# Kernel tuning notes

Hardware: AMD Instinct MI355X
Metric: run time of the kernel (lower is better)

## Reference

```python
import jax, jax.numpy as jnp
import numpy as np

EPS = 1e-5

def _batchnorm(x, gamma, beta):
    # x: [N, C, T]; training-mode BN: batch stats over (N, T) per channel
    mean = jnp.mean(x, axis=(0, 2), keepdims=True)
    var = jnp.mean((x - mean) ** 2, axis=(0, 2), keepdims=True)
    xhat = (x - mean) * jax.lax.rsqrt(var + EPS)
    return xhat * gamma[None, :, None] + beta[None, :, None]

def _temporal_shift(x, s):
    # x: [N, C, T], s: [C] learnable per-channel shift (Shift-GCN style)
    # out[n,c,t] = linear interp of x[n,c, t + s[c]], zero outside [0, T)
    N, C, T = x.shape
    pos = jnp.arange(T, dtype=x.dtype)[None, :] + s[:, None]  # [C, T]
    i0f = jnp.floor(pos)
    frac = pos - i0f                                          # [C, T]
    i0 = i0f.astype(jnp.int32)
    i1 = i0 + 1
    v0 = ((i0 >= 0) & (i0 < T)).astype(x.dtype)
    v1 = ((i1 >= 0) & (i1 < T)).astype(x.dtype)
    cidx = jnp.arange(C)[:, None]                             # [C, 1]
    g0 = x[:, cidx, jnp.clip(i0, 0, T - 1)]                   # [N, C, T]
    g1 = x[:, cidx, jnp.clip(i1, 0, T - 1)]
    return g0 * ((1.0 - frac) * v0) + g1 * (frac * v1)

def setup_inputs() -> dict:
    key = jax.random.key(0)
    ks = jax.random.split(key, 5)
    N, T, Cin, Cout = 128, 1024, 256, 256
    x = jax.random.normal(ks[0], (N, T, Cin), dtype=jnp.float32)
    # kaiming_normal fan_out for 1x1 conv: std = sqrt(2 / Cout)
    conv_w = jax.random.normal(ks[1], (Cout, Cin), dtype=jnp.float32) * np.sqrt(2.0 / Cout)
    conv_b = jnp.zeros((Cout,), dtype=jnp.float32)
    shift_in_s = jax.random.uniform(ks[2], (Cin,), dtype=jnp.float32, minval=-1.0, maxval=1.0)
    shift_out_s = jax.random.uniform(ks[3], (Cout,), dtype=jnp.float32, minval=-1.0, maxval=1.0)
    return {
        "x": x,
        "bn1_gamma": jnp.ones((Cin,), jnp.float32),
        "bn1_beta": jnp.zeros((Cin,), jnp.float32),
        "shift_in_s": shift_in_s,
        "conv_w": conv_w,
        "conv_b": conv_b,
        "shift_out_s": shift_out_s,
        "bn2_gamma": jnp.ones((Cout,), jnp.float32),
        "bn2_beta": jnp.zeros((Cout,), jnp.float32),
    }

def reference(x, bn1_gamma, bn1_beta, shift_in_s, conv_w, conv_b, shift_out_s, bn2_gamma, bn2_beta):
    # x: [N, T, C] -> [N, C, T] (permute; trailing singleton W dim elided)
    h = jnp.transpose(x, (0, 2, 1))
    h = _batchnorm(h, bn1_gamma, bn1_beta)
    h = _temporal_shift(h, shift_in_s)
    # 1x1 conv == per-position channel mixing
    h = jnp.einsum("nct,oc->not", h, conv_w) + conv_b[None, :, None]
    h = jax.nn.relu(h)
    h = _temporal_shift(h, shift_out_s)
    h = _batchnorm(h, bn2_gamma, bn2_beta)
    return jnp.transpose(h, (0, 2, 1))  # back to [N, T, C_out]
```

## Files before the change

### kernel.cpp

```cpp
#include <hip/hip_runtime.h>
#include <stddef.h>

typedef __attribute__((ext_vector_type(8))) short short8;
typedef __attribute__((ext_vector_type(4))) float f32x4;
typedef __attribute__((ext_vector_type(4))) int   i32x4;
typedef __attribute__((ext_vector_type(2))) unsigned int u32x2;
typedef unsigned short ushort_t;
typedef unsigned int uint_t;

#define TT 1024
#define NT 131072.0f
#define EPS 1e-5f

__device__ __forceinline__ float bf2f(ushort_t u){
    union { float f; uint_t i; } v; v.i = ((uint_t)u) << 16; return v.f;
}
__device__ __forceinline__ ushort_t f2bf(float f){
    union { float f; uint_t i; } v; v.f = f;
    uint_t r = v.i + 0x7fffu + ((v.i >> 16) & 1u);
    return (ushort_t)(r >> 16);
}
__device__ __forceinline__ uint_t pack2(float lo, float hi){
    return (uint_t)f2bf(lo) | ((uint_t)f2bf(hi) << 16);
}
__device__ __forceinline__ f32x4 ld4bf(const ushort_t* p){
    u32x2 u = *(const u32x2*)p;
    f32x4 r;
    r[0] = bf2f((ushort_t)(u[0] & 0xffffu));
    r[1] = bf2f((ushort_t)(u[0] >> 16));
    r[2] = bf2f((ushort_t)(u[1] & 0xffffu));
    r[3] = bf2f((ushort_t)(u[1] >> 16));
    return r;
}
__device__ __forceinline__ void wave_red(float& v){
    #pragma unroll
    for (int off = 32; off > 0; off >>= 1) v += __shfl_down(v, off);
}
__device__ __forceinline__ void dma16(const void* g, void* l){
    __builtin_amdgcn_global_load_lds(
        (const __attribute__((address_space(1))) unsigned int*)g,
        (__attribute__((address_space(3))) unsigned int*)l, 16, 0, 0);
}

__global__ __launch_bounds__(256) void k_prep(const float* __restrict__ x,
                                              const float* __restrict__ a0i,
                                              const float* __restrict__ a1i,
                                              const int* __restrict__ i1i,
                                              ushort_t* __restrict__ xs,
                                              float* __restrict__ psum,
                                              float* __restrict__ psq){
    __shared__ float ls[4][256], lq[4][256];
    const int b = blockIdx.x, tid = threadIdx.x;
    const int c4 = (tid & 63) << 2, rq = tid >> 6;
    const size_t row0 = ((size_t)b << 6) + ((size_t)rq << 4);
    const int n = (int)(row0 >> 10), rt = (int)(row0 & 1023);
    const float* xp = x + ((size_t)n << 18) + c4;
    ushort_t* wp = xs + ((size_t)n << 18);
    const f32x4 a0v = *(const f32x4*)&a0i[c4];
    const f32x4 a1v = *(const f32x4*)&a1i[c4];
    const i32x4 i1v = *(const i32x4*)&i1i[c4];
    f32x4 s = {0.f,0.f,0.f,0.f}, q = {0.f,0.f,0.f,0.f};
    f32x4 Bm1 = {0.f,0.f,0.f,0.f};
    if (rt > 0) Bm1 = *(const f32x4*)&xp[(size_t)(rt - 1) << 8];
    f32x4 B0 = *(const f32x4*)&xp[(size_t)rt << 8];
    #pragma unroll 8
    for (int k = 0; k < 16; ++k){
        const int t = rt + k;
        f32x4 Bp1 = {0.f,0.f,0.f,0.f};
        if (t < 1023) Bp1 = *(const f32x4*)&xp[(size_t)(t + 1) << 8];
        f32x4 v;
        #pragma unroll
        for (int j = 0; j < 4; ++j){
            s[j] += B0[j]; q[j] = fmaf(B0[j], B0[j], q[j]);
            float zl = i1v[j] ? B0[j]  : Bm1[j];
            float zr = i1v[j] ? Bp1[j] : B0[j];
            v[j] = a0v[j] * zl + a1v[j] * zr;
        }
        u32x2 u; u[0] = pack2(v[0], v[1]); u[1] = pack2(v[2], v[3]);
        *(u32x2*)&wp[((size_t)t << 8) + (c4 ^ ((t & 7) << 3))] = u;
        Bm1 = B0; B0 = Bp1;
    }
    #pragma unroll
    for (int j = 0; j < 4; ++j){ ls[rq][c4 + j] = s[j]; lq[rq][c4 + j] = q[j]; }
    __syncthreads();
    const int c = tid;
    psum[(size_t)b * 256 + c] = ls[0][c] + ls[1][c] + ls[2][c] + ls[3][c];
    psq [(size_t)b * 256 + c] = lq[0][c] + lq[1][c] + lq[2][c] + lq[3][c];
}

__global__ __launch_bounds__(256) void k_shift(const float* __restrict__ sin_,
                                               const float* __restrict__ sout,
                                               float* __restrict__ a0i, float* __restrict__ a1i,
                                               int* __restrict__ i1i,
                                               float* __restrict__ a0o, float* __restrict__ a1o,
                                               int* __restrict__ j1o){
    const int c = blockIdx.x * 256 + threadIdx.x;
    if (c < 256){
        float sv = sin_[c]; float fi = floorf(sv); float fr = sv - fi;
        a0i[c] = 1.f - fr; a1i[c] = fr; i1i[c] = (int)fi + 1;
        float so = sout[c]; float fo = floorf(so); float fro = so - fo;
        a0o[c] = 1.f - fro; a1o[c] = fro; j1o[c] = (int)fo + 1;
    }
}

__global__ __launch_bounds__(256) void k_fin1(const float* __restrict__ psum,
                                              const float* __restrict__ psq,
                                              const float* __restrict__ g1,
                                              const float* __restrict__ be1,
                                              float* __restrict__ s1, float* __restrict__ b1){
    const int c = blockIdx.x, t = threadIdx.x;
    float s = 0.f, q = 0.f;
    #pragma unroll
    for (int i = 0; i < 8; ++i){
        const size_t b = (size_t)(t * 8 + i);
        s += psum[b * 256 + c]; q += psq[b * 256 + c];
    }
    wave_red(s); wave_red(q);
    __shared__ float sm[8];
    const int wv = t >> 6, ln = t & 63;
    if (ln == 0){ sm[wv] = s; sm[4 + wv] = q; }
    __syncthreads();
    if (t == 0){
        float S = sm[0] + sm[1] + sm[2] + sm[3];
        float Q = sm[4] + sm[5] + sm[6] + sm[7];
        float mean = S / NT;
        float var  = Q / NT - mean * mean;
        float rstd = rsqrtf(var + EPS);
        float sc = rstd * g1[c];
        s1[c] = sc;
        b1[c] = be1[c] - mean * sc;
    }
}

__global__ __launch_bounds__(256) void k_wf(const float* __restrict__ W,
                                            const float* __restrict__ s1,
                                            ushort_t* __restrict__ WF){
    const int gid = blockIdx.x * 256 + threadIdx.x;
    const int l = gid & 63, ob = (gid >> 6) & 15, ks = gid >> 10;
    const int row = ob * 16 + (l & 15);
    const int k0  = ks * 32 + (l >> 4) * 8;
    #pragma unroll
    for (int j = 0; j < 8; ++j)
        WF[(size_t)gid * 8 + j] = f2bf(W[(size_t)row * 256 + k0 + j] * s1[k0 + j]);
}

__global__ __launch_bounds__(256) void k_wb(const float* __restrict__ W,
                                            const float* __restrict__ cb,
                                            const float* __restrict__ b1,
                                            const float* __restrict__ a0i,
                                            const float* __restrict__ a1i,
                                            const int* __restrict__ i1i,
                                            float* __restrict__ bias2,
                                            float* __restrict__ corr0,
                                            float* __restrict__ corrT){
    const int o = blockIdx.x, c = threadIdx.x;
    const float w = W[(size_t)o * 256 + c];
    float wb = w * b1[c];
    float c0 = (i1i[c] == 0) ? wb * a0i[c] : 0.f;
    float cT = (i1i[c] == 1) ? wb * a1i[c] : 0.f;
    wave_red(wb); wave_red(c0); wave_red(cT);
    __shared__ float sm[4][3];
    const int wv = c >> 6, ln = c & 63;
    if (ln == 0){ sm[wv][0] = wb; sm[wv][1] = c0; sm[wv][2] = cT; }
    __syncthreads();
    if (c == 0){
        bias2[o] = cb[o] + sm[0][0] + sm[1][0] + sm[2][0] + sm[3][0];
        corr0[o] = sm[0][1] + sm[1][1] + sm[2][1] + sm[3][1];
        corrT[o] = sm[0][2] + sm[1][2] + sm[2][2] + sm[3][2];
    }
}

__global__ __launch_bounds__(256) void k_conv(const ushort_t* __restrict__ xs,
                                              const ushort_t* __restrict__ WF,
                                              const float* __restrict__ bias2,
                                              const float* __restrict__ corr0,
                                              const float* __restrict__ corrT,
                                              ushort_t* __restrict__ Y,
                                              float* __restrict__ SP, float* __restrict__ SQ,
                                              float* __restrict__ SR,
                                              float* __restrict__ FR, float* __restrict__ LR){
    __shared__ __align__(16) ushort_t lds[16384];
    const int tid = threadIdx.x;
    const int n  = blockIdx.x >> 4;
    const int t0 = (blockIdx.x & 15) << 6;
    const int lane = tid & 63, wv = tid >> 6;

    {
        const ushort_t* gsrc = xs + ((size_t)n << 18) + ((size_t)(t0 + (wv << 4)) << 8);
        #pragma unroll
        for (int i = 0; i < 8; ++i)
            dma16(gsrc + (i << 9) + (lane << 3), &lds[(wv << 12) + (i << 9)]);
    }
    __syncthreads();

    const int l15 = lane & 15, lg = lane >> 4;
    f32x4 acc[4][4];
    #pragma unroll
    for (int r = 0; r < 4; ++r)
        #pragma unroll
        for (int q = 0; q < 4; ++q)
            acc[r][q] = (f32x4){0.f, 0.f, 0.f, 0.f};

    const short8* wf8 = (const short8*)WF;
    #pragma unroll
    for (int ks = 0; ks < 8; ++ks){
        short8 aF[4], bF[4];
        #pragma unroll
        for (int r = 0; r < 4; ++r)
            aF[r] = wf8[(ks * 16 + wv * 4 + r) * 64 + lane];
        const int kk = (ks << 5) + (lg << 3);
        #pragma unroll
        for (int q = 0; q < 4; ++q){
            const int t = (q << 4) | l15;
            bF[q] = *(const short8*)&lds[(t << 8) + (kk ^ ((t & 7) << 3))];
        }
        #pragma unroll
        for (int r = 0; r < 4; ++r)
            #pragma unroll
            for (int q = 0; q < 4; ++q)
                acc[r][q] = __builtin_amdgcn_mfma_f32_16x16x32_bf16(aF[r], bF[q], acc[r][q], 0, 0, 0);
    }
    __syncthreads();

    const bool isFirst = (t0 == 0), isLast = (t0 == 960);
    #pragma unroll
    for (int r = 0; r < 4; ++r){
        const int ob = (wv << 6) + (r << 4) + (lg << 2);
        const f32x4 cbv = *(const f32x4*)&bias2[ob];
        f32x4 c0v = {0.f,0.f,0.f,0.f}, cTv = {0.f,0.f,0.f,0.f};
        if (isFirst) c0v = *(const f32x4*)&corr0[ob];
        if (isLast)  cTv = *(const f32x4*)&corrT[ob];
        #pragma unroll
        for (int q = 0; q < 4; ++q){
            const int t = (q << 4) | l15;
            float v[4];
            #pragma unroll
            for (int j = 0; j < 4; ++j){
                float z = acc[r][q][j] + cbv[j];
                if (isFirst && t == 0)  z -= c0v[j];
                if (isLast  && t == 63) z -= cTv[j];
                v[j] = z > 0.f ? z : 0.f;
            }
            u32x2 w; w[0] = pack2(v[0], v[1]); w[1] = pack2(v[2], v[3]);
            *(u32x2*)&lds[(t << 8) + (ob ^ ((t & 7) << 3))] = w;
        }
    }
    __syncthreads();

    u32x2* Yu = (u32x2*)Y;
    const size_t rbase = ((size_t)n << 10) + t0;
    #pragma unroll
    for (int it = 0; it < 16; ++it){
        const int row = (it << 2) + wv;
        u32x2 v = *(const u32x2*)&lds[(row << 8) + ((lane << 2) ^ ((row & 7) << 3))];
        Yu[((rbase + row) << 6) + lane] = v;
    }
    {
        const int o = tid;
        FR[(size_t)blockIdx.x * 256 + o] = bf2f(lds[o]);
        LR[(size_t)blockIdx.x * 256 + o] = bf2f(lds[(63 << 8) + (o ^ 56)]);
    }
    f32x4 P = {0.f,0.f,0.f,0.f}, Q = P, R = P;
    {
        const int o4 = lane << 2;
        const int r0 = wv << 4;
        f32x4 prev = {0.f,0.f,0.f,0.f};
        if (wv > 0) prev = ld4bf(&lds[((r0 - 1) << 8) + (o4 ^ (((r0 - 1) & 7) << 3))]);
        #pragma unroll 8
        for (int k = 0; k < 16; ++k){
            const int t = r0 + k;
            f32x4 y = ld4bf(&lds[(t << 8) + (o4 ^ ((t & 7) << 3))]);
            #pragma unroll
            for (int j = 0; j < 4; ++j){
                P[j] += y[j];
                Q[j] = fmaf(y[j], y[j], Q[j]);
                R[j] = fmaf(prev[j], y[j], R[j]);
            }
            prev = y;
        }
    }
    __syncthreads();
    float* fl = (float*)lds;
    {
        const int o4 = lane << 2;
        *(f32x4*)&fl[wv * 768 + o4]       = P;
        *(f32x4*)&fl[wv * 768 + 256 + o4] = Q;
        *(f32x4*)&fl[wv * 768 + 512 + o4] = R;
    }
    __syncthreads();
    {
        const int o = tid;
        float p = fl[o] + fl[768 + o] + fl[1536 + o] + fl[2304 + o];
        float q = fl[256 + o] + fl[1024 + o] + fl[1792 + o] + fl[2560 + o];
        float r = fl[512 + o] + fl[1280 + o] + fl[2048 + o] + fl[2816 + o];
        const size_t idx = (size_t)blockIdx.x * 256 + o;
        SP[idx] = p; SQ[idx] = q; SR[idx] = r;
    }
}

__global__ __launch_bounds__(256) void k_fin2(const float* __restrict__ SP,
                                              const float* __restrict__ SQ,
                                              const float* __restrict__ SR,
                                              const float* __restrict__ FR,
                                              const float* __restrict__ LR,
                                              const float* __restrict__ g2,
                                              const float* __restrict__ be2,
                                              const float* __restrict__ a0o,
                                              const float* __restrict__ a1o,
                                              const int* __restrict__ j1o,
                                              float* __restrict__ s2, float* __restrict__ b2){
    const int o = blockIdx.x, t = threadIdx.x;
    float P = 0.f, Q = 0.f, R = 0.f, b0p = 0.f, b0q = 0.f, btp = 0.f, btq = 0.f;
    #pragma unroll
    for (int i = 0; i < 8; ++i){
        const int b = t * 8 + i;
        const size_t idx = (size_t)b * 256 + o;
        P += SP[idx]; Q += SQ[idx];
        float r = SR[idx];
        const float fr = FR[idx], lr = LR[idx];
        const int tile = b & 15;
        if (tile > 0) r = fmaf(LR[idx - 256], fr, r);
        R += r;
        if (tile == 0){ b0p += fr; b0q += fr * fr; }
        if (tile == 15){ btp += lr; btq += lr * lr; }
    }
    wave_red(P); wave_red(Q); wave_red(R);
    wave_red(b0p); wave_red(b0q); wave_red(btp); wave_red(btq);
    __shared__ float sm[4][7];
    const int wv = t >> 6, ln = t & 63;
    if (ln == 0){
        sm[wv][0] = P; sm[wv][1] = Q; sm[wv][2] = R;
        sm[wv][3] = b0p; sm[wv][4] = b0q; sm[wv][5] = btp; sm[wv][6] = btq;
    }
    __syncthreads();
    if (t == 0){
        float v[7];
        #pragma unroll
        for (int k = 0; k < 7; ++k)
            v[k] = sm[0][k] + sm[1][k] + sm[2][k] + sm[3][k];
        const float a0 = a0o[o], a1 = a1o[o];
        const int j1 = j1o[o];
        float sz, sq;
        if (j1 == 0){
            sz = a0 * (v[0] - v[5]) + a1 * v[0];
            sq = a0 * a0 * (v[1] - v[6]) + a1 * a1 * v[1] + 2.f * a0 * a1 * v[2];
        } else {
            sz = a0 * v[0] + a1 * (v[0] - v[3]);
            sq = a0 * a0 * v[1] + a1 * a1 * (v[1] - v[4]) + 2.f * a0 * a1 * v[2];
        }
        float mean = sz / NT;
        float var  = sq / NT - mean * mean;
        float rstd = rsqrtf(var + EPS);
        float sc = rstd * g2[o];
        s2[o] = sc;
        b2[o] = be2[o] - mean * sc;
    }
}

__global__ __launch_bounds__(256) void k_out(const ushort_t* __restrict__ Y,
                                             const float* __restrict__ s2,
                                             const float* __restrict__ b2,
                                             const float* __restrict__ a0o,
                                             const float* __restrict__ a1o,
                                             const int* __restrict__ j1o,
                                             float* __restrict__ out){
    const int b = blockIdx.x, tid = threadIdx.x;
    const int n = b >> 4, o4 = (tid & 63) << 2, rq = tid >> 6;
    const int rs = ((b & 15) << 6) + (rq << 4);
    const f32x4 sc = *(const f32x4*)&s2[o4];
    const f32x4 bs = *(const f32x4*)&b2[o4];
    const f32x4 a0 = *(const f32x4*)&a0o[o4];
    const f32x4 a1 = *(const f32x4*)&a1o[o4];
    const i32x4 j1 = *(const i32x4*)&j1o[o4];
    const ushort_t* yb = Y + ((size_t)n << 18) + o4;
    float* ob = out + ((size_t)n << 18) + o4;
    f32x4 ym1 = {0.f,0.f,0.f,0.f};
    if (rs > 0) ym1 = ld4bf(yb + ((size_t)(rs - 1) << 8));
    f32x4 y0 = ld4bf(yb + ((size_t)rs << 8));
    #pragma unroll 8
    for (int k = 0; k < 16; ++k){
        const int t = rs + k;
        f32x4 yp1 = {0.f,0.f,0.f,0.f};
        if (t < 1023) yp1 = ld4bf(yb + ((size_t)(t + 1) << 8));
        f32x4 ov;
        #pragma unroll
        for (int j = 0; j < 4; ++j){
            float zl = j1[j] ? y0[j]  : ym1[j];
            float zr = j1[j] ? yp1[j] : y0[j];
            float z = a0[j] * zl + a1[j] * zr;
            ov[j] = fmaf(z, sc[j], bs[j]);
        }
        *(f32x4*)&ob[(size_t)t << 8] = ov;
        ym1 = y0; y0 = yp1;
    }
}

extern "C" void kernel_launch(void* const* d_in, const int* in_sizes, int n_in,
                              void* d_out, int out_size, void* d_ws, size_t ws_size,
                              hipStream_t stream){
    const float* x    = (const float*)d_in[0];
    const float* g1   = (const float*)d_in[1];
    const float* be1  = (const float*)d_in[2];
    const float* sin_ = (const float*)d_in[3];
    const float* W    = (const float*)d_in[4];
    const float* cb   = (const float*)d_in[5];
    const float* sout = (const float*)d_in[6];
    const float* g2   = (const float*)d_in[7];
    const float* be2  = (const float*)d_in[8];
    float* out = (float*)d_out;

    char* ws = (char*)d_ws;
    ushort_t* Y  = (ushort_t*)ws;
    ushort_t* WF = (ushort_t*)(ws + 67108864);
    float* SP = (float*)(ws + 67239936);
    float* SQ = SP + 524288;
    float* SR = SQ + 524288;
    float* FR = SR + 524288;
    float* LR = FR + 524288;
    float* par = LR + 524288;
    float* s1    = par;         float* b1    = par + 256;
    float* a0i   = par + 512;   float* a1i   = par + 768;
    int*   i1i   = (int*)(par + 1024);
    float* a0o   = par + 1280;  float* a1o   = par + 1536;
    int*   j1o   = (int*)(par + 1792);
    float* s2    = par + 2048;  float* b2    = par + 2304;
    float* bias2 = par + 2560;  float* corr0 = par + 2816;
    float* corrT = par + 3072;
    float* psum = (float*)ws;
    float* psq  = psum + 524288;
    ushort_t* xs = (ushort_t*)d_out;

    k_shift<<<1, 256, 0, stream>>>(sin_, sout, a0i, a1i, i1i, a0o, a1o, j1o);
    k_prep <<<2048, 256, 0, stream>>>(x, a0i, a1i, i1i, xs, psum, psq);
    k_fin1 <<<256, 256, 0, stream>>>(psum, psq, g1, be1, s1, b1);
    k_wf   <<<32, 256, 0, stream>>>(W, s1, WF);
    k_wb   <<<256, 256, 0, stream>>>(W, cb, b1, a0i, a1i, i1i, bias2, corr0, corrT);
    k_conv <<<2048, 256, 0, stream>>>(xs, WF, bias2, corr0, corrT,
                                      Y, SP, SQ, SR, FR, LR);
    k_fin2 <<<256, 256, 0, stream>>>(SP, SQ, SR, FR, LR,
                                     g2, be2, a0o, a1o, j1o, s2, b2);
    k_out  <<<2048, 256, 0, stream>>>(Y, s2, b2, a0o, a1o, j1o, out);
}
```

Before: 162.2 us.

## Fold shift-param kernels into consumers, merge weight prep, widen prep/out to 8 channels

New measurement: 156.6 us. 3.5% less time.

```diff
diff --git a/kernel.cpp b/kernel.cpp
--- a/kernel.cpp
+++ b/kernel.cpp
@@ -3,8 +3,8 @@
 
 typedef __attribute__((ext_vector_type(8))) short short8;
 typedef __attribute__((ext_vector_type(4))) float f32x4;
-typedef __attribute__((ext_vector_type(4))) int   i32x4;
 typedef __attribute__((ext_vector_type(2))) unsigned int u32x2;
+typedef __attribute__((ext_vector_type(4))) unsigned int u32x4;
 typedef unsigned short ushort_t;
 typedef unsigned int uint_t;
 
@@ -32,6 +32,13 @@
     r[3] = bf2f((ushort_t)(u[1] >> 16));
     return r;
 }
+__device__ __forceinline__ void ld8bf(const ushort_t* p, f32x4& lo, f32x4& hi){
+    u32x4 u = *(const u32x4*)p;
+    lo[0] = bf2f((ushort_t)(u[0] & 0xffffu)); lo[1] = bf2f((ushort_t)(u[0] >> 16));
+    lo[2] = bf2f((ushort_t)(u[1] & 0xffffu)); lo[3] = bf2f((ushort_t)(u[1] >> 16));
+    hi[0] = bf2f((ushort_t)(u[2] & 0xffffu)); hi[1] = bf2f((ushort_t)(u[2] >> 16));
+    hi[2] = bf2f((ushort_t)(u[3] & 0xffffu)); hi[3] = bf2f((ushort_t)(u[3] >> 16));
+}
 __device__ __forceinline__ void wave_red(float& v){
     #pragma unroll
     for (int off = 32; off > 0; off >>= 1) v += __shfl_down(v, off);
@@ -43,64 +50,69 @@
 }
 
 __global__ __launch_bounds__(256) void k_prep(const float* __restrict__ x,
-                                              const float* __restrict__ a0i,
-                                              const float* __restrict__ a1i,
-                                              const int* __restrict__ i1i,
+                                              const float* __restrict__ sin_,
                                               ushort_t* __restrict__ xs,
                                               float* __restrict__ psum,
                                               float* __restrict__ psq){
-    __shared__ float ls[4][256], lq[4][256];
+    __shared__ float ls[8][256], lq[8][256];
     const int b = blockIdx.x, tid = threadIdx.x;
-    const int c4 = (tid & 63) << 2, rq = tid >> 6;
-    const size_t row0 = ((size_t)b << 6) + ((size_t)rq << 4);
+    const int c8 = (tid & 31) << 3, rg = tid >> 5;
+    const size_t row0 = ((size_t)b << 6) + ((size_t)rg << 3);
     const int n = (int)(row0 >> 10), rt = (int)(row0 & 1023);
-    const float* xp = x + ((size_t)n << 18) + c4;
+    const float* xp = x + ((size_t)n << 18) + c8;
     ushort_t* wp = xs + ((size_t)n << 18);
-    const f32x4 a0v = *(const f32x4*)&a0i[c4];
-    const f32x4 a1v = *(const f32x4*)&a1i[c4];
-    const i32x4 i1v = *(const i32x4*)&i1i[c4];
-    f32x4 s = {0.f,0.f,0.f,0.f}, q = {0.f,0.f,0.f,0.f};
-    f32x4 Bm1 = {0.f,0.f,0.f,0.f};
-    if (rt > 0) Bm1 = *(const f32x4*)&xp[(size_t)(rt - 1) << 8];
-    f32x4 B0 = *(const f32x4*)&xp[(size_t)rt << 8];
-    #pragma unroll 8
-    for (int k = 0; k < 16; ++k){
+    float a0[8], a1[8]; int i1[8];
+    #pragma unroll
+    for (int j = 0; j < 8; ++j){
+        float sv = sin_[c8 + j]; float fi = floorf(sv); float fr = sv - fi;
+        a0[j] = 1.f - fr; a1[j] = fr; i1[j] = (int)fi + 1;
+    }
+    f32x4 s0 = {0.f,0.f,0.f,0.f}, s1v = s0, q0 = s0, q1 = s0;
+    f32x4 Am = s0, Bm = s0, A0 = s0, B0 = s0;
+    if (rt > 0){
+        Am = *(const f32x4*)&xp[(size_t)(rt - 1) << 8];
+        Bm = *(const f32x4*)&xp[((size_t)(rt - 1) << 8) + 4];
+    }
+    A0 = *(const f32x4*)&xp[(size_t)rt << 8];
+    B0 = *(const f32x4*)&xp[((size_t)rt << 8) + 4];
+    #pragma unroll
+    for (int k = 0; k < 8; ++k){
         const int t = rt + k;
-        f32x4 Bp1 = {0.f,0.f,0.f,0.f};
-        if (t < 1023) Bp1 = *(const f32x4*)&xp[(size_t)(t + 1) << 8];
-        f32x4 v;
+        f32x4 Ap = {0.f,0.f,0.f,0.f}, Bp = Ap;
+        if (t < 1023){
+            Ap = *(const f32x4*)&xp[(size_t)(t + 1) << 8];
+            Bp = *(const f32x4*)&xp[((size_t)(t + 1) << 8) + 4];
+        }
+        float v[8];
         #pragma unroll
         for (int j = 0; j < 4; ++j){
-            s[j] += B0[j]; q[j] = fmaf(B0[j], B0[j], q[j]);
-            float zl = i1v[j] ? B0[j]  : Bm1[j];
-            float zr = i1v[j] ? Bp1[j] : B0[j];
-            v[j] = a0v[j] * zl + a1v[j] * zr;
-        }
-        u32x2 u; u[0] = pack2(v[0], v[1]); u[1] = pack2(v[2], v[3]);
-        *(u32x2*)&wp[((size_t)t << 8) + (c4 ^ ((t & 7) << 3))] = u;
-        Bm1 = B0; B0 = Bp1;
-    }
-    #pragma unroll
-    for (int j = 0; j < 4; ++j){ ls[rq][c4 + j] = s[j]; lq[rq][c4 + j] = q[j]; }
+            s0[j] += A0[j]; q0[j] = fmaf(A0[j], A0[j], q0[j]);
+            s1v[j] += B0[j]; q1[j] = fmaf(B0[j], B0[j], q1[j]);
+            float zl = i1[j] ? A0[j] : Am[j];
+            float zr = i1[j] ? Ap[j] : A0[j];
+            v[j] = a0[j] * zl + a1[j] * zr;
+            float zl2 = i1[4 + j] ? B0[j] : Bm[j];
+            float zr2 = i1[4 + j] ? Bp[j] : B0[j];
+            v[4 + j] = a0[4 + j] * zl2 + a1[4 + j] * zr2;
+        }
+        u32x4 u;
+        u[0] = pack2(v[0], v[1]); u[1] = pack2(v[2], v[3]);
+        u[2] = pack2(v[4], v[5]); u[3] = pack2(v[6], v[7]);
+        *(u32x4*)&wp[((size_t)t << 8) + (c8 ^ ((t & 7) << 3))] = u;
+        Am = A0; Bm = B0; A0 = Ap; B0 = Bp;
+    }
+    #pragma unroll
+    for (int j = 0; j < 4; ++j){
+        ls[rg][c8 + j] = s0[j];     lq[rg][c8 + j] = q0[j];
+        ls[rg][c8 + 4 + j] = s1v[j]; lq[rg][c8 + 4 + j] = q1[j];
+    }
     __syncthreads();
     const int c = tid;
-    psum[(size_t)b * 256 + c] = ls[0][c] + ls[1][c] + ls[2][c] + ls[3][c];
-    psq [(size_t)b * 256 + c] = lq[0][c] + lq[1][c] + lq[2][c] + lq[3][c];
-}
-
-__global__ __launch_bounds__(256) void k_shift(const float* __restrict__ sin_,
-                                               const float* __restrict__ sout,
-                                               float* __restrict__ a0i, float* __restrict__ a1i,
-                                               int* __restrict__ i1i,
-                                               float* __restrict__ a0o, float* __restrict__ a1o,
-                                               int* __restrict__ j1o){
-    const int c = blockIdx.x * 256 + threadIdx.x;
-    if (c < 256){
-        float sv = sin_[c]; float fi = floorf(sv); float fr = sv - fi;
-        a0i[c] = 1.f - fr; a1i[c] = fr; i1i[c] = (int)fi + 1;
-        float so = sout[c]; float fo = floorf(so); float fro = so - fo;
-        a0o[c] = 1.f - fro; a1o[c] = fro; j1o[c] = (int)fo + 1;
-    }
+    float ps = 0.f, pq = 0.f;
+    #pragma unroll
+    for (int g = 0; g < 8; ++g){ ps += ls[g][c]; pq += lq[g][c]; }
+    psum[(size_t)b * 256 + c] = ps;
+    psq [(size_t)b * 256 + c] = pq;
 }
 
 __global__ __launch_bounds__(256) void k_fin1(const float* __restrict__ psum,
@@ -132,32 +144,24 @@
     }
 }
 
-__global__ __launch_bounds__(256) void k_wf(const float* __restrict__ W,
-                                            const float* __restrict__ s1,
-                                            ushort_t* __restrict__ WF){
-    const int gid = blockIdx.x * 256 + threadIdx.x;
-    const int l = gid & 63, ob = (gid >> 6) & 15, ks = gid >> 10;
-    const int row = ob * 16 + (l & 15);
-    const int k0  = ks * 32 + (l >> 4) * 8;
-    #pragma unroll
-    for (int j = 0; j < 8; ++j)
-        WF[(size_t)gid * 8 + j] = f2bf(W[(size_t)row * 256 + k0 + j] * s1[k0 + j]);
-}
-
-__global__ __launch_bounds__(256) void k_wb(const float* __restrict__ W,
-                                            const float* __restrict__ cb,
-                                            const float* __restrict__ b1,
-                                            const float* __restrict__ a0i,
-                                            const float* __restrict__ a1i,
-                                            const int* __restrict__ i1i,
-                                            float* __restrict__ bias2,
-                                            float* __restrict__ corr0,
-                                            float* __restrict__ corrT){
+__global__ __launch_bounds__(256) void k_w(const float* __restrict__ W,
+                                           const float* __restrict__ cb,
+                                           const float* __restrict__ s1,
+                                           const float* __restrict__ b1,
+                                           const float* __restrict__ sin_,
+                                           ushort_t* __restrict__ WF,
+                                           float* __restrict__ bias2,
+                                           float* __restrict__ corr0,
+                                           float* __restrict__ corrT){
     const int o = blockIdx.x, c = threadIdx.x;
     const float w = W[(size_t)o * 256 + c];
+    float sv = sin_[c]; float fi = floorf(sv); float fr = sv - fi;
+    const float a0 = 1.f - fr, a1 = fr; const int i1 = (int)fi + 1;
+    const int ks = c >> 5, lg = (c & 31) >> 3, j = c & 7;
+    WF[(size_t)(((ks * 16 + (o >> 4)) * 64 + lg * 16 + (o & 15)) * 8 + j)] = f2bf(w * s1[c]);
     float wb = w * b1[c];
-    float c0 = (i1i[c] == 0) ? wb * a0i[c] : 0.f;
-    float cT = (i1i[c] == 1) ? wb * a1i[c] : 0.f;
+    float c0 = (i1 == 0) ? wb * a0 : 0.f;
+    float cT = (i1 == 1) ? wb * a1 : 0.f;
     wave_red(wb); wave_red(c0); wave_red(cT);
     __shared__ float sm[4][3];
     const int wv = c >> 6, ln = c & 63;
@@ -305,9 +309,7 @@
                                               const float* __restrict__ LR,
                                               const float* __restrict__ g2,
                                               const float* __restrict__ be2,
-                                              const float* __restrict__ a0o,
-                                              const float* __restrict__ a1o,
-                                              const int* __restrict__ j1o,
+                                              const float* __restrict__ sout,
                                               float* __restrict__ s2, float* __restrict__ b2){
     const int o = blockIdx.x, t = threadIdx.x;
     float P = 0.f, Q = 0.f, R = 0.f, b0p = 0.f, b0q = 0.f, btp = 0.f, btq = 0.f;
@@ -338,8 +340,9 @@
         #pragma unroll
         for (int k = 0; k < 7; ++k)
             v[k] = sm[0][k] + sm[1][k] + sm[2][k] + sm[3][k];
-        const float a0 = a0o[o], a1 = a1o[o];
-        const int j1 = j1o[o];
+        float so = sout[o]; float fo = floorf(so); float fro = so - fo;
+        const float a0 = 1.f - fro, a1 = fro;
+        const int j1 = (int)fo + 1;
         float sz, sq;
         if (j1 == 0){
             sz = a0 * (v[0] - v[5]) + a1 * v[0];
@@ -360,38 +363,41 @@
 __global__ __launch_bounds__(256) void k_out(const ushort_t* __restrict__ Y,
                                              const float* __restrict__ s2,
                                              const float* __restrict__ b2,
-                                             const float* __restrict__ a0o,
-                                             const float* __restrict__ a1o,
-                                             const int* __restrict__ j1o,
+                                             const float* __restrict__ sout,
                                              float* __restrict__ out){
     const int b = blockIdx.x, tid = threadIdx.x;
-    const int n = b >> 4, o4 = (tid & 63) << 2, rq = tid >> 6;
-    const int rs = ((b & 15) << 6) + (rq << 4);
-    const f32x4 sc = *(const f32x4*)&s2[o4];
-    const f32x4 bs = *(const f32x4*)&b2[o4];
-    const f32x4 a0 = *(const f32x4*)&a0o[o4];
-    const f32x4 a1 = *(const f32x4*)&a1o[o4];
-    const i32x4 j1 = *(const i32x4*)&j1o[o4];
-    const ushort_t* yb = Y + ((size_t)n << 18) + o4;
-    float* ob = out + ((size_t)n << 18) + o4;
-    f32x4 ym1 = {0.f,0.f,0.f,0.f};
-    if (rs > 0) ym1 = ld4bf(yb + ((size_t)(rs - 1) << 8));
-    f32x4 y0 = ld4bf(yb + ((size_t)rs << 8));
-    #pragma unroll 8
-    for (int k = 0; k < 16; ++k){
+    const int n = b >> 4, c8 = (tid & 31) << 3, rg = tid >> 5;
+    const int rs = ((b & 15) << 6) + (rg << 3);
+    float sc[8], bs[8], a0[8], a1[8]; int j1[8];
+    #pragma unroll
+    for (int j = 0; j < 8; ++j){
+        sc[j] = s2[c8 + j]; bs[j] = b2[c8 + j];
+        float so = sout[c8 + j]; float fo = floorf(so); float fro = so - fo;
+        a0[j] = 1.f - fro; a1[j] = fro; j1[j] = (int)fo + 1;
+    }
+    const ushort_t* yb = Y + ((size_t)n << 18) + c8;
+    float* ob = out + ((size_t)n << 18) + c8;
+    f32x4 m0 = {0.f,0.f,0.f,0.f}, m1 = m0, z0, z1;
+    if (rs > 0) ld8bf(yb + ((size_t)(rs - 1) << 8), m0, m1);
+    ld8bf(yb + ((size_t)rs << 8), z0, z1);
+    #pragma unroll
+    for (int k = 0; k < 8; ++k){
         const int t = rs + k;
-        f32x4 yp1 = {0.f,0.f,0.f,0.f};
-        if (t < 1023) yp1 = ld4bf(yb + ((size_t)(t + 1) << 8));
-        f32x4 ov;
+        f32x4 p0 = {0.f,0.f,0.f,0.f}, p1 = p0;
+        if (t < 1023) ld8bf(yb + ((size_t)(t + 1) << 8), p0, p1);
+        f32x4 o0, o1;
         #pragma unroll
         for (int j = 0; j < 4; ++j){
-            float zl = j1[j] ? y0[j]  : ym1[j];
-            float zr = j1[j] ? yp1[j] : y0[j];
-            float z = a0[j] * zl + a1[j] * zr;
-            ov[j] = fmaf(z, sc[j], bs[j]);
-        }
-        *(f32x4*)&ob[(size_t)t << 8] = ov;
-        ym1 = y0; y0 = yp1;
+            float zl = j1[j] ? z0[j] : m0[j];
+            float zr = j1[j] ? p0[j] : z0[j];
+            o0[j] = fmaf(a0[j] * zl + a1[j] * zr, sc[j], bs[j]);
+            float zl2 = j1[4 + j] ? z1[j] : m1[j];
+            float zr2 = j1[4 + j] ? p1[j] : z1[j];
+            o1[j] = fmaf(a0[4 + j] * zl2 + a1[4 + j] * zr2, sc[4 + j], bs[4 + j]);
+        }
+        *(f32x4*)&ob[(size_t)t << 8] = o0;
+        *(f32x4*)&ob[((size_t)t << 8) + 4] = o1;
+        m0 = z0; m1 = z1; z0 = p0; z1 = p1;
     }
 }
 
@@ -419,25 +425,19 @@
     float* LR = FR + 524288;
     float* par = LR + 524288;
     float* s1    = par;         float* b1    = par + 256;
-    float* a0i   = par + 512;   float* a1i   = par + 768;
-    int*   i1i   = (int*)(par + 1024);
-    float* a0o   = par + 1280;  float* a1o   = par + 1536;
-    int*   j1o   = (int*)(par + 1792);
-    float* s2    = par + 2048;  float* b2    = par + 2304;
-    float* bias2 = par + 2560;  float* corr0 = par + 2816;
-    float* corrT = par + 3072;
+    float* s2    = par + 512;   float* b2    = par + 768;
+    float* bias2 = par + 1024;  float* corr0 = par + 1280;
+    float* corrT = par + 1536;
     float* psum = (float*)ws;
     float* psq  = psum + 524288;
     ushort_t* xs = (ushort_t*)d_out;
 
-    k_shift<<<1, 256, 0, stream>>>(sin_, sout, a0i, a1i, i1i, a0o, a1o, j1o);
-    k_prep <<<2048, 256, 0, stream>>>(x, a0i, a1i, i1i, xs, psum, psq);
+    k_prep <<<2048, 256, 0, stream>>>(x, sin_, xs, psum, psq);
     k_fin1 <<<256, 256, 0, stream>>>(psum, psq, g1, be1, s1, b1);
-    k_wf   <<<32, 256, 0, stream>>>(W, s1, WF);
-    k_wb   <<<256, 256, 0, stream>>>(W, cb, b1, a0i, a1i, i1i, bias2, corr0, corrT);
+    k_w    <<<256, 256, 0, stream>>>(W, cb, s1, b1, sin_, WF, bias2, corr0, corrT);
     k_conv <<<2048, 256, 0, stream>>>(xs, WF, bias2, corr0, corrT,
                                       Y, SP, SQ, SR, FR, LR);
     k_fin2 <<<256, 256, 0, stream>>>(SP, SQ, SR, FR, LR,
-                                     g2, be2, a0o, a1o, j1o, s2, b2);
-    k_out  <<<2048, 256, 0, stream>>>(Y, s2, b2, a0o, a1o, j1o, out);
-}
+                                     g2, be2, sout, s2, b2);
+    k_out  <<<2048, 256, 0, stream>>>(Y, s2, b2, sout, out);
+}
```
